# Performance work log

Measured on AMD Instinct MI355X. Metric: run time of the kernel, lower is better.

The kernel has to match this reference:

```python
import jax, jax.numpy as jnp
import numpy as np

BS, D = 8192, 128
SIGMA = 16.0

def setup_inputs() -> dict:
    key = jax.random.key(0)
    x = jax.random.normal(key, (BS, D), dtype=jnp.float32)
    return {"x": x}

def reference(x) -> jnp.ndarray:
    # kernel[j, i] = exp(-||x_i - x_j||^2 / (2 sigma^2))  (symmetric RBF Gram matrix)
    # Computed via the ||a-b||^2 = |a|^2 + |b|^2 - 2 a.b GEMM trick instead of the
    # original O(bs) loop of slice/sub/sum ops (same math, fused form).
    sq = jnp.sum(x * x, axis=1)                      # [bs]
    d2 = sq[:, None] + sq[None, :] - 2.0 * (x @ x.T)  # [bs, bs]
    d2 = jnp.maximum(d2, 0.0)                         # clamp tiny negative fp error
    kernel = jnp.exp(-d2 / (2.0 * SIGMA * SIGMA))
    # symmetric degree normalization: D^{-1/2} K D^{-1/2}
    ds = 1.0 / jnp.sqrt(jnp.sum(kernel, axis=0))      # [bs]
    return kernel * (ds[:, None] * ds[None, :])
```

## Files before the change

### kernel.cpp

```cpp
#include <hip/hip_runtime.h>
#include <hip/hip_bf16.h>

#define BSZ 8192
#define DIM 128

typedef __attribute__((ext_vector_type(8))) short bf16x8;
typedef __attribute__((ext_vector_type(4))) float f32x4;

__device__ __forceinline__ ushort f32_to_bf16(float f) {
    unsigned u = __float_as_uint(f);
    u += 0x7FFF + ((u >> 16) & 1);
    return (ushort)(u >> 16);
}

__global__ __launch_bounds__(256) void prep_kernel(const float* __restrict__ x,
                                                   ushort* __restrict__ xb,
                                                   float* __restrict__ sq) {
    const int wid  = threadIdx.x >> 6;
    const int lane = threadIdx.x & 63;
    const int row  = blockIdx.x * 4 + wid;
    const float2 v = *reinterpret_cast<const float2*>(x + (size_t)row * DIM + lane * 2);
    float s = v.x * v.x + v.y * v.y;
    #pragma unroll
    for (int off = 32; off; off >>= 1) s += __shfl_down(s, off);
    if (lane == 0) sq[row] = s;
    ushort2 b;
    b.x = f32_to_bf16(v.x);
    b.y = f32_to_bf16(v.y);
    *reinterpret_cast<ushort2*>(xb + (size_t)row * DIM + lane * 2) = b;
}

template <int PHASE>
__global__ __launch_bounds__(256) void rbf_kernel(const ushort* __restrict__ xb,
                                                  const float* __restrict__ sq,
                                                  float* __restrict__ colsum,
                                                  float* __restrict__ out) {
    const int lane = threadIdx.x & 63;
    const int wid  = threadIdx.x >> 6;
    const int fr   = lane & 15;
    const int kg   = lane >> 4;

    const int bx = blockIdx.x & 63;
    const int by = blockIdx.x >> 6;
    const int row0 = by * 128 + (wid >> 1) * 64;
    const int col0 = bx * 128 + (wid & 1) * 64;

    f32x4 acc[4][4];
    #pragma unroll
    for (int mi = 0; mi < 4; ++mi)
        #pragma unroll
        for (int ni = 0; ni < 4; ++ni)
            acc[mi][ni] = (f32x4){0.f, 0.f, 0.f, 0.f};

    #pragma unroll
    for (int kk = 0; kk < 4; ++kk) {
        const int ko = kk * 32 + kg * 8;
        bf16x8 a[4], b[4];
        #pragma unroll
        for (int mi = 0; mi < 4; ++mi)
            a[mi] = *reinterpret_cast<const bf16x8*>(xb + (size_t)(row0 + mi * 16 + fr) * DIM + ko);
        #pragma unroll
        for (int ni = 0; ni < 4; ++ni)
            b[ni] = *reinterpret_cast<const bf16x8*>(xb + (size_t)(col0 + ni * 16 + fr) * DIM + ko);
        #pragma unroll
        for (int mi = 0; mi < 4; ++mi)
            #pragma unroll
            for (int ni = 0; ni < 4; ++ni)
                acc[mi][ni] = __builtin_amdgcn_mfma_f32_16x16x32_bf16(a[mi], b[ni], acc[mi][ni], 0, 0, 0);
    }

    float sqr[4][4];
    #pragma unroll
    for (int mi = 0; mi < 4; ++mi) {
        const f32x4 t = *reinterpret_cast<const f32x4*>(sq + row0 + mi * 16 + kg * 4);
        #pragma unroll
        for (int r = 0; r < 4; ++r) sqr[mi][r] = t[r];
    }
    float sqc[4];
    #pragma unroll
    for (int ni = 0; ni < 4; ++ni) sqc[ni] = sq[col0 + ni * 16 + fr];

    const float inv = 1.0f / 512.0f;

    if (PHASE == 0) {
        float csum[4] = {0.f, 0.f, 0.f, 0.f};
        #pragma unroll
        for (int mi = 0; mi < 4; ++mi)
            #pragma unroll
            for (int ni = 0; ni < 4; ++ni)
                #pragma unroll
                for (int r = 0; r < 4; ++r) {
                    float t = fminf((2.f * acc[mi][ni][r] - sqr[mi][r] - sqc[ni]) * inv, 0.f);
                    csum[ni] += __expf(t);
                }
        #pragma unroll
        for (int ni = 0; ni < 4; ++ni) {
            csum[ni] += __shfl_xor(csum[ni], 16);
            csum[ni] += __shfl_xor(csum[ni], 32);
        }
        if (lane < 16) {
            #pragma unroll
            for (int ni = 0; ni < 4; ++ni)
                atomicAdd(&colsum[col0 + ni * 16 + fr], csum[ni]);
        }
    } else {
        float dsc[4];
        #pragma unroll
        for (int ni = 0; ni < 4; ++ni) dsc[ni] = rsqrtf(colsum[col0 + ni * 16 + fr]);
        float dsr[4][4];
        #pragma unroll
        for (int mi = 0; mi < 4; ++mi) {
            const f32x4 t = *reinterpret_cast<const f32x4*>(colsum + row0 + mi * 16 + kg * 4);
            #pragma unroll
            for (int r = 0; r < 4; ++r) dsr[mi][r] = rsqrtf(t[r]);
        }
        #pragma unroll
        for (int mi = 0; mi < 4; ++mi)
            #pragma unroll
            for (int ni = 0; ni < 4; ++ni)
                #pragma unroll
                for (int r = 0; r < 4; ++r) {
                    float t = fminf((2.f * acc[mi][ni][r] - sqr[mi][r] - sqc[ni]) * inv, 0.f);
                    float k = __expf(t);
                    const int row = row0 + mi * 16 + kg * 4 + r;
                    const int col = col0 + ni * 16 + fr;
                    out[(size_t)row * BSZ + col] = k * dsr[mi][r] * dsc[ni];
                }
    }
}

extern "C" void kernel_launch(void* const* d_in, const int* in_sizes, int n_in,
                              void* d_out, int out_size, void* d_ws, size_t ws_size,
                              hipStream_t stream) {
    const float* x = (const float*)d_in[0];
    float* out = (float*)d_out;

    ushort* xb    = (ushort*)d_ws;
    float* sq     = (float*)((char*)d_ws + (size_t)BSZ * DIM * 2);
    float* colsum = sq + BSZ;

    hipMemsetAsync(colsum, 0, BSZ * sizeof(float), stream);
    prep_kernel<<<BSZ / 4, 256, 0, stream>>>(x, xb, sq);
    rbf_kernel<0><<<64 * 64, 256, 0, stream>>>(xb, sq, colsum, out);
    rbf_kernel<1><<<64 * 64, 256, 0, stream>>>(xb, sq, colsum, out);
}
```

Before: 362.8 us.

## Pre-swizzle bf16 operands into MFMA fragment order and use nontemporal output stores

The prep kernel now writes the bf16 copy of x in a fragment-major layout, where each 16-row group and k-slice forms a contiguous 64-lane by 8-element block. Each MFMA operand load in the GEMM kernel then becomes one fully coalesced 1KB wavefront read instead of 16 strided row reads. The prep kernel processes 16 rows per wave with float4 loads, and its grid shrinks to match. The normalized output is written with nontemporal stores so the 256MB result does not pollute the caches.

Result: faster. 325.5 us (-10.3%).

```diff
diff --git a/kernel.cpp b/kernel.cpp
--- a/kernel.cpp
+++ b/kernel.cpp
@@ -18,16 +18,29 @@
                                                    float* __restrict__ sq) {
     const int wid  = threadIdx.x >> 6;
     const int lane = threadIdx.x & 63;
-    const int row  = blockIdx.x * 4 + wid;
-    const float2 v = *reinterpret_cast<const float2*>(x + (size_t)row * DIM + lane * 2);
-    float s = v.x * v.x + v.y * v.y;
+    const int g    = blockIdx.x * 4 + wid;
+    const int fr   = lane & 15;
+    const int kg   = lane >> 4;
+    const int row  = g * 16 + fr;
+
+    float s = 0.f;
     #pragma unroll
-    for (int off = 32; off; off >>= 1) s += __shfl_down(s, off);
-    if (lane == 0) sq[row] = s;
-    ushort2 b;
-    b.x = f32_to_bf16(v.x);
-    b.y = f32_to_bf16(v.y);
-    *reinterpret_cast<ushort2*>(xb + (size_t)row * DIM + lane * 2) = b;
+    for (int kk = 0; kk < 4; ++kk) {
+        const float* p = x + (size_t)row * DIM + kk * 32 + kg * 8;
+        const float4 v0 = *reinterpret_cast<const float4*>(p);
+        const float4 v1 = *reinterpret_cast<const float4*>(p + 4);
+        s += v0.x * v0.x + v0.y * v0.y + v0.z * v0.z + v0.w * v0.w;
+        s += v1.x * v1.x + v1.y * v1.y + v1.z * v1.z + v1.w * v1.w;
+        bf16x8 b;
+        b[0] = (short)f32_to_bf16(v0.x); b[1] = (short)f32_to_bf16(v0.y);
+        b[2] = (short)f32_to_bf16(v0.z); b[3] = (short)f32_to_bf16(v0.w);
+        b[4] = (short)f32_to_bf16(v1.x); b[5] = (short)f32_to_bf16(v1.y);
+        b[6] = (short)f32_to_bf16(v1.z); b[7] = (short)f32_to_bf16(v1.w);
+        *reinterpret_cast<bf16x8*>(xb + ((size_t)(g * 4 + kk) * 64 + lane) * 8) = b;
+    }
+    s += __shfl_xor(s, 16);
+    s += __shfl_xor(s, 32);
+    if (lane < 16) sq[row] = s;
 }
 
 template <int PHASE>
@@ -44,6 +57,8 @@
     const int by = blockIdx.x >> 6;
     const int row0 = by * 128 + (wid >> 1) * 64;
     const int col0 = bx * 128 + (wid & 1) * 64;
+    const int ga = row0 >> 4;
+    const int gb = col0 >> 4;
 
     f32x4 acc[4][4];
     #pragma unroll
@@ -54,14 +69,15 @@
 
     #pragma unroll
     for (int kk = 0; kk < 4; ++kk) {
-        const int ko = kk * 32 + kg * 8;
         bf16x8 a[4], b[4];
         #pragma unroll
         for (int mi = 0; mi < 4; ++mi)
-            a[mi] = *reinterpret_cast<const bf16x8*>(xb + (size_t)(row0 + mi * 16 + fr) * DIM + ko);
+            a[mi] = *reinterpret_cast<const bf16x8*>(
+                xb + ((size_t)((ga + mi) * 4 + kk) * 64 + lane) * 8);
         #pragma unroll
         for (int ni = 0; ni < 4; ++ni)
-            b[ni] = *reinterpret_cast<const bf16x8*>(xb + (size_t)(col0 + ni * 16 + fr) * DIM + ko);
+            b[ni] = *reinterpret_cast<const bf16x8*>(
+                xb + ((size_t)((gb + ni) * 4 + kk) * 64 + lane) * 8);
         #pragma unroll
         for (int mi = 0; mi < 4; ++mi)
             #pragma unroll
@@ -124,7 +140,8 @@
                     float k = __expf(t);
                     const int row = row0 + mi * 16 + kg * 4 + r;
                     const int col = col0 + ni * 16 + fr;
-                    out[(size_t)row * BSZ + col] = k * dsr[mi][r] * dsc[ni];
+                    __builtin_nontemporal_store(k * dsr[mi][r] * dsc[ni],
+                                                &out[(size_t)row * BSZ + col]);
                 }
     }
 }
@@ -140,7 +157,7 @@
     float* colsum = sq + BSZ;
 
     hipMemsetAsync(colsum, 0, BSZ * sizeof(float), stream);
-    prep_kernel<<<BSZ / 4, 256, 0, stream>>>(x, xb, sq);
+    prep_kernel<<<512 / 4, 256, 0, stream>>>(x, xb, sq);
     rbf_kernel<0><<<64 * 64, 256, 0, stream>>>(xb, sq, colsum, out);
     rbf_kernel<1><<<64 * 64, 256, 0, stream>>>(xb, sq, colsum, out);
 }
```
